# Performance work log

Hardware: AMD Instinct MI355X
Metric: run time of the kernel (lower is better)

The kernel has to match this reference:

```python
import jax, jax.numpy as jnp
import numpy as np

B, H, W, D = 64, 32, 32, 64
K = 1024  # codebook_size


def setup_inputs() -> dict:
    key = jax.random.key(0)
    kz, ke = jax.random.split(key)
    z = jax.random.normal(kz, (B, H, W, D), dtype=jnp.float32)
    embeddings = 0.02 * jax.random.normal(ke, (K, D), dtype=jnp.float32)
    return {"z": z, "embeddings": embeddings}


def reference(z, embeddings):
    # Flatten spatial/batch dims: (N, D) with N = B*H*W
    z_flat = z.reshape(-1, z.shape[-1])
    # Squared euclidean distances via ||a||^2 + ||b||^2 - 2 a.b  -> (N, K)
    distances = (jnp.sum(z_flat ** 2, axis=1, keepdims=True)
                 + jnp.sum(embeddings ** 2, axis=1)
                 - 2.0 * jnp.dot(z_flat, embeddings.T))
    indices = jnp.argmin(distances, axis=1)  # (N,)
    quantized = embeddings[indices].reshape(z.shape)  # (B, H, W, D)
    indices = indices.reshape(z.shape[0], z.shape[1], z.shape[2])  # (B, H, W)
    return quantized, indices
```

## Files before the change

kernel.cpp:

```cpp
#include <hip/hip_runtime.h>

#define NPTS   65536
#define DDIM   64
#define KCODES 1024
#define QOUT_ELEMS (NPTS * DDIM)

typedef _Float16 half8    __attribute__((ext_vector_type(8)));
typedef float    floatx16 __attribute__((ext_vector_type(16)));
typedef unsigned int uint;

#define AS1 __attribute__((address_space(1)))
#define AS3 __attribute__((address_space(3)))

#define WS_EHP   0
#define WS_ELP   (128*1024)
#define WS_E2    (256*1024)
#define WS_SCR   (264*1024)

union H8U { half8 v; uint u[4]; };

static __device__ __forceinline__ void gl_lds16(const void* g, void* l) {
    __builtin_amdgcn_global_load_lds((const AS1 uint*)g, (AS3 uint*)l, 16, 0, 0);
}

__global__ void eprep_kernel(const float* __restrict__ emb, char* __restrict__ ws) {
    const int tid = threadIdx.x;
    const int w = tid >> 6, d = tid & 63;
    const int k = blockIdx.x * 4 + w;
    float v = emb[(size_t)k * DDIM + d];
    _Float16 h = (_Float16)v;
    _Float16 l = (_Float16)(v - (float)h);
    size_t off = (size_t)(k >> 5) * 4096 + (size_t)(d >> 3) * 512
               + (size_t)(k & 31) * 16 + (size_t)(d & 7) * 2;
    *(_Float16*)(ws + WS_EHP + off) = h;
    *(_Float16*)(ws + WS_ELP + off) = l;
    float s = v * v;
    #pragma unroll
    for (int m = 1; m < 64; m <<= 1) s += __shfl_xor(s, m, 64);
    if (d == 0) {
        _Float16 e2h = (_Float16)s;
        _Float16 e2l = (_Float16)(s - (float)e2h);
        unsigned short hb = *(unsigned short*)&e2h;
        unsigned short lb = *(unsigned short*)&e2l;
        ((uint*)(ws + WS_E2))[k] = (uint)hb | ((uint)lb << 16);
    }
}

__global__ __launch_bounds__(256, 3) void vq_kernel(
    const float* __restrict__ z,
    const char* __restrict__ ws_c,
    float2* __restrict__ scr)
{
    const int tid  = threadIdx.x;
    const int lane = tid & 63;
    const int w    = __builtin_amdgcn_readfirstlane(tid >> 6);
    const int col  = lane & 31;
    const int sel8 = lane >> 5;
    const int pgrp = blockIdx.x >> 2;
    const int kq   = blockIdx.x & 3;

    __shared__ uint4 ldsbuf[2][512];
    __shared__ uint  lds_e2[256];

    const int pt = pgrp * 128 + w * 32 + col;
    half8 ah[4], al[4];
    {
        const float* zrow = z + (size_t)pt * DDIM + sel8 * 8;
        #pragma unroll
        for (int ks = 0; ks < 4; ++ks) {
            float4 u0 = *(const float4*)(zrow + ks * 16);
            float4 u1 = *(const float4*)(zrow + ks * 16 + 4);
            float tv[8] = {u0.x, u0.y, u0.z, u0.w, u1.x, u1.y, u1.z, u1.w};
            #pragma unroll
            for (int j = 0; j < 8; ++j) {
                float a = -2.0f * tv[j];
                _Float16 hh = (_Float16)a;
                ah[ks][j] = hh;
                al[ks][j] = (_Float16)(a - (float)hh);
            }
        }
    }
    half8 ahE;
    { H8U t0; t0.u[0] = (sel8 == 0) ? 0x3C003C00u : 0u;
      t0.u[1] = t0.u[2] = t0.u[3] = 0u; ahE = t0.v; }

    if (w == 0)
        gl_lds16(ws_c + WS_E2 + kq * 1024 + lane * 16, (char*)lds_e2);
    {
        const int opnd = w >> 1, hf = w & 1;
        const char* src = ws_c + (opnd ? WS_ELP : WS_EHP)
                        + (size_t)(kq * 8) * 4096 + hf * 2048 + lane * 16;
        char* dst = (char*)ldsbuf[0] + opnd * 4096 + hf * 2048;
        gl_lds16(src, dst);
        gl_lds16(src + 1024, dst + 1024);
    }

    const floatx16 zeroC = {};
    float best[16];
    int   bt[16];
    #pragma unroll
    for (int r = 0; r < 16; ++r) { best[r] = 3.4e38f; bt[r] = 0; }

    for (int t = 0; t < 8; ++t) {
        __syncthreads();
        if (t < 7) {
            const int opnd = w >> 1, hf = w & 1;
            const char* src = ws_c + (opnd ? WS_ELP : WS_EHP)
                            + (size_t)(kq * 8 + t + 1) * 4096 + hf * 2048 + lane * 16;
            char* dst = (char*)ldsbuf[(t + 1) & 1] + opnd * 4096 + hf * 2048;
            gl_lds16(src, dst);
            gl_lds16(src + 1024, dst + 1024);
        }
        const char* buf = (const char*)ldsbuf[t & 1];
        const char* ehb = buf + sel8 * 512 + col * 16;
        const char* elb = ehb + 4096;
        half8 bh[4], bl[4];
        #pragma unroll
        for (int ks = 0; ks < 4; ++ks) {
            bh[ks] = *(const half8*)(ehb + ks * 1024);
            bl[ks] = *(const half8*)(elb + ks * 1024);
        }
        half8 bhE;
        { H8U u; u.u[0] = lds_e2[t * 32 + col];
          u.u[1] = u.u[2] = u.u[3] = 0u; bhE = u.v; }

        floatx16 acc;
        acc = __builtin_amdgcn_mfma_f32_32x32x16_f16(ah[0], bh[0], zeroC, 0, 0, 0);
        acc = __builtin_amdgcn_mfma_f32_32x32x16_f16(ah[1], bh[1], acc, 0, 0, 0);
        acc = __builtin_amdgcn_mfma_f32_32x32x16_f16(ah[2], bh[2], acc, 0, 0, 0);
        acc = __builtin_amdgcn_mfma_f32_32x32x16_f16(ah[3], bh[3], acc, 0, 0, 0);
        acc = __builtin_amdgcn_mfma_f32_32x32x16_f16(ahE,  bhE,  acc, 0, 0, 0);
        acc = __builtin_amdgcn_mfma_f32_32x32x16_f16(ah[0], bl[0], acc, 0, 0, 0);
        acc = __builtin_amdgcn_mfma_f32_32x32x16_f16(ah[1], bl[1], acc, 0, 0, 0);
        acc = __builtin_amdgcn_mfma_f32_32x32x16_f16(ah[2], bl[2], acc, 0, 0, 0);
        acc = __builtin_amdgcn_mfma_f32_32x32x16_f16(ah[3], bl[3], acc, 0, 0, 0);
        acc = __builtin_amdgcn_mfma_f32_32x32x16_f16(al[0], bh[0], acc, 0, 0, 0);
        acc = __builtin_amdgcn_mfma_f32_32x32x16_f16(al[1], bh[1], acc, 0, 0, 0);
        acc = __builtin_amdgcn_mfma_f32_32x32x16_f16(al[2], bh[2], acc, 0, 0, 0);
        acc = __builtin_amdgcn_mfma_f32_32x32x16_f16(al[3], bh[3], acc, 0, 0, 0);

        #pragma unroll
        for (int r = 0; r < 16; ++r) {
            bool c = acc[r] < best[r];
            best[r] = c ? acc[r] : best[r];
            bt[r]   = c ? t      : bt[r];
        }
    }

    int code[16];
    #pragma unroll
    for (int r = 0; r < 16; ++r) code[r] = kq * 256 + bt[r] * 32 + col;
    #pragma unroll
    for (int m = 1; m < 32; m <<= 1) {
        #pragma unroll
        for (int r = 0; r < 16; ++r) {
            float ov = __shfl_xor(best[r], m, 64);
            int   oc = __shfl_xor(code[r], m, 64);
            bool c = (ov < best[r]) || (ov == best[r] && oc < code[r]);
            best[r] = c ? ov : best[r];
            code[r] = c ? oc : code[r];
        }
    }
    if (col == 0) {
        #pragma unroll
        for (int r = 0; r < 16; ++r) {
            int row = (r & 3) + 8 * (r >> 2) + 4 * sel8;
            int p = pgrp * 128 + w * 32 + row;
            scr[(size_t)p * 4 + kq] = make_float2(best[r], __int_as_float(code[r]));
        }
    }
}

__global__ void merge_gather_kernel(const float* __restrict__ emb,
                                    const float2* __restrict__ scr,
                                    float* __restrict__ out)
{
    int f = blockIdx.x * 256 + threadIdx.x;
    int pt = f >> 4, d4 = f & 15;
    float2 c0 = scr[(size_t)pt * 4];
    float bv = c0.x; int bi = __float_as_int(c0.y);
    #pragma unroll
    for (int j = 1; j < 4; ++j) {
        float2 cj = scr[(size_t)pt * 4 + j];
        if (cj.x < bv) { bv = cj.x; bi = __float_as_int(cj.y); }
    }
    ((float4*)out)[(size_t)pt * 16 + d4] = ((const float4*)emb)[(size_t)bi * 16 + d4];
    if (d4 == 0) out[QOUT_ELEMS + pt] = (float)bi;
}

extern "C" void kernel_launch(void* const* d_in, const int* in_sizes, int n_in,
                              void* d_out, int out_size, void* d_ws, size_t ws_size,
                              hipStream_t stream) {
    const float* z   = (const float*)d_in[0];
    const float* emb = (const float*)d_in[1];
    float* out = (float*)d_out;
    char* ws = (char*)d_ws;
    float2* scr = (float2*)(ws + WS_SCR);

    eprep_kernel<<<KCODES / 4, 256, 0, stream>>>(emb, ws);
    vq_kernel<<<2048, 256, 0, stream>>>(z, ws, scr);
    merge_gather_kernel<<<NPTS * 16 / 256, 256, 0, stream>>>(emb, scr, out);
}
```

Before: 118.0 us.

## Swap MFMA operand roles: keep codebook slice in registers, stream points through LDS

A new zprep kernel pre-splits -2z into fp16 hi/lo pairs in an MFMA-friendly tiled layout. The main kernel now holds a 128-code slice of the codebook in registers and streams 256 points through double-buffered LDS, not the other way round. The ||e||^2 term becomes a plain fp32 register add instead of an extra MFMA. The argmin is now reduced inside each thread's accumulator rows, with one cross-half shuffle and an LDS merge across waves, replacing the 5-step shuffle reduction. The cost is an extra pass that writes and rereads 16 MB of z halves, an 8-way candidate merge per point, and a reworked gather kernel.

Result: no change. 117.8 us (-0.2%).

```diff
diff --git a/kernel.cpp b/kernel.cpp
--- a/kernel.cpp
+++ b/kernel.cpp
@@ -14,10 +14,10 @@
 
 #define WS_EHP   0
 #define WS_ELP   (128*1024)
-#define WS_E2    (256*1024)
-#define WS_SCR   (264*1024)
-
-union H8U { half8 v; uint u[4]; };
+#define WS_E2F   (256*1024)
+#define WS_ZH    (512*1024)
+#define WS_ZL    (WS_ZH + 8*1024*1024)
+#define WS_SCR   (WS_ZH + 16*1024*1024)
 
 static __device__ __forceinline__ void gl_lds16(const void* g, void* l) {
     __builtin_amdgcn_global_load_lds((const AS1 uint*)g, (AS3 uint*)l, 16, 0, 0);
@@ -37,17 +37,23 @@
     float s = v * v;
     #pragma unroll
     for (int m = 1; m < 64; m <<= 1) s += __shfl_xor(s, m, 64);
-    if (d == 0) {
-        _Float16 e2h = (_Float16)s;
-        _Float16 e2l = (_Float16)(s - (float)e2h);
-        unsigned short hb = *(unsigned short*)&e2h;
-        unsigned short lb = *(unsigned short*)&e2l;
-        ((uint*)(ws + WS_E2))[k] = (uint)hb | ((uint)lb << 16);
-    }
+    if (d == 0) ((float*)(ws + WS_E2F))[k] = s;
+}
+
+__global__ void zprep_kernel(const float* __restrict__ z, char* __restrict__ ws) {
+    const int tid = threadIdx.x;
+    const int w = tid >> 6, d = tid & 63;
+    const int p = blockIdx.x * 4 + w;
+    float a = -2.0f * z[(size_t)p * DDIM + d];
+    _Float16 h = (_Float16)a;
+    _Float16 l = (_Float16)(a - (float)h);
+    size_t off = (size_t)(p >> 5) * 4096 + (size_t)(d >> 3) * 512
+               + (size_t)(p & 31) * 16 + (size_t)(d & 7) * 2;
+    *(_Float16*)(ws + WS_ZH + off) = h;
+    *(_Float16*)(ws + WS_ZL + off) = l;
 }
 
 __global__ __launch_bounds__(256, 3) void vq_kernel(
-    const float* __restrict__ z,
     const char* __restrict__ ws_c,
     float2* __restrict__ scr)
 {
@@ -56,80 +62,76 @@
     const int w    = __builtin_amdgcn_readfirstlane(tid >> 6);
     const int col  = lane & 31;
     const int sel8 = lane >> 5;
-    const int pgrp = blockIdx.x >> 2;
-    const int kq   = blockIdx.x & 3;
-
-    __shared__ uint4 ldsbuf[2][512];
-    __shared__ uint  lds_e2[256];
-
-    const int pt = pgrp * 128 + w * 32 + col;
+    const int pgrp = blockIdx.x >> 3;
+    const int kg   = blockIdx.x & 7;
+
+    __shared__ uint4  zbuf[2][512];
+    __shared__ float2 cand[2][4][32];
+
+    const char* eb = ws_c + WS_EHP + (size_t)(kg * 4 + w) * 4096 + sel8 * 512 + col * 16;
     half8 ah[4], al[4];
+    #pragma unroll
+    for (int ks = 0; ks < 4; ++ks) {
+        ah[ks] = *(const half8*)(eb + ks * 1024);
+        al[ks] = *(const half8*)(eb + (WS_ELP - WS_EHP) + ks * 1024);
+    }
+    float e2r[16];
     {
-        const float* zrow = z + (size_t)pt * DDIM + sel8 * 8;
-        #pragma unroll
-        for (int ks = 0; ks < 4; ++ks) {
-            float4 u0 = *(const float4*)(zrow + ks * 16);
-            float4 u1 = *(const float4*)(zrow + ks * 16 + 4);
-            float tv[8] = {u0.x, u0.y, u0.z, u0.w, u1.x, u1.y, u1.z, u1.w};
-            #pragma unroll
-            for (int j = 0; j < 8; ++j) {
-                float a = -2.0f * tv[j];
-                _Float16 hh = (_Float16)a;
-                ah[ks][j] = hh;
-                al[ks][j] = (_Float16)(a - (float)hh);
-            }
-        }
-    }
-    half8 ahE;
-    { H8U t0; t0.u[0] = (sel8 == 0) ? 0x3C003C00u : 0u;
-      t0.u[1] = t0.u[2] = t0.u[3] = 0u; ahE = t0.v; }
-
-    if (w == 0)
-        gl_lds16(ws_c + WS_E2 + kq * 1024 + lane * 16, (char*)lds_e2);
+        const float* e2f = (const float*)(ws_c + WS_E2F) + kg * 128 + w * 32 + 4 * sel8;
+        #pragma unroll
+        for (int r = 0; r < 16; ++r)
+            e2r[r] = e2f[(r & 3) + 8 * (r >> 2)];
+    }
+
     {
         const int opnd = w >> 1, hf = w & 1;
-        const char* src = ws_c + (opnd ? WS_ELP : WS_EHP)
-                        + (size_t)(kq * 8) * 4096 + hf * 2048 + lane * 16;
-        char* dst = (char*)ldsbuf[0] + opnd * 4096 + hf * 2048;
+        const char* src = ws_c + (opnd ? WS_ZL : WS_ZH)
+                        + (size_t)(pgrp * 8) * 4096 + hf * 2048 + lane * 16;
+        char* dst = (char*)zbuf[0] + opnd * 4096 + hf * 2048;
         gl_lds16(src, dst);
         gl_lds16(src + 1024, dst + 1024);
     }
 
     const floatx16 zeroC = {};
-    float best[16];
-    int   bt[16];
-    #pragma unroll
-    for (int r = 0; r < 16; ++r) { best[r] = 3.4e38f; bt[r] = 0; }
 
     for (int t = 0; t < 8; ++t) {
         __syncthreads();
         if (t < 7) {
             const int opnd = w >> 1, hf = w & 1;
-            const char* src = ws_c + (opnd ? WS_ELP : WS_EHP)
-                            + (size_t)(kq * 8 + t + 1) * 4096 + hf * 2048 + lane * 16;
-            char* dst = (char*)ldsbuf[(t + 1) & 1] + opnd * 4096 + hf * 2048;
+            const char* src = ws_c + (opnd ? WS_ZL : WS_ZH)
+                            + (size_t)(pgrp * 8 + t + 1) * 4096 + hf * 2048 + lane * 16;
+            char* dst = (char*)zbuf[(t + 1) & 1] + opnd * 4096 + hf * 2048;
             gl_lds16(src, dst);
             gl_lds16(src + 1024, dst + 1024);
         }
-        const char* buf = (const char*)ldsbuf[t & 1];
-        const char* ehb = buf + sel8 * 512 + col * 16;
-        const char* elb = ehb + 4096;
+        if (t > 0 && w == ((t - 1) & 3) && lane < 32) {
+            const int tt = t - 1;
+            float2 c0 = cand[tt & 1][0][lane];
+            float bvm = c0.x; int bim = __float_as_int(c0.y);
+            #pragma unroll
+            for (int j = 1; j < 4; ++j) {
+                float2 cj = cand[tt & 1][j][lane];
+                bool c = cj.x < bvm;
+                bvm = c ? cj.x : bvm;
+                bim = c ? __float_as_int(cj.y) : bim;
+            }
+            int ptg = (pgrp * 8 + tt) * 32 + lane;
+            scr[(size_t)ptg * 8 + kg] = make_float2(bvm, __int_as_float(bim));
+        }
+
+        const char* zb = (const char*)zbuf[t & 1] + sel8 * 512 + col * 16;
         half8 bh[4], bl[4];
         #pragma unroll
         for (int ks = 0; ks < 4; ++ks) {
-            bh[ks] = *(const half8*)(ehb + ks * 1024);
-            bl[ks] = *(const half8*)(elb + ks * 1024);
-        }
-        half8 bhE;
-        { H8U u; u.u[0] = lds_e2[t * 32 + col];
-          u.u[1] = u.u[2] = u.u[3] = 0u; bhE = u.v; }
+            bh[ks] = *(const half8*)(zb + ks * 1024);
+            bl[ks] = *(const half8*)(zb + 4096 + ks * 1024);
+        }
 
         floatx16 acc;
         acc = __builtin_amdgcn_mfma_f32_32x32x16_f16(ah[0], bh[0], zeroC, 0, 0, 0);
         acc = __builtin_amdgcn_mfma_f32_32x32x16_f16(ah[1], bh[1], acc, 0, 0, 0);
         acc = __builtin_amdgcn_mfma_f32_32x32x16_f16(ah[2], bh[2], acc, 0, 0, 0);
         acc = __builtin_amdgcn_mfma_f32_32x32x16_f16(ah[3], bh[3], acc, 0, 0, 0);
-        acc = __builtin_amdgcn_mfma_f32_32x32x16_f16(ahE,  bhE,  acc, 0, 0, 0);
         acc = __builtin_amdgcn_mfma_f32_32x32x16_f16(ah[0], bl[0], acc, 0, 0, 0);
         acc = __builtin_amdgcn_mfma_f32_32x32x16_f16(ah[1], bl[1], acc, 0, 0, 0);
         acc = __builtin_amdgcn_mfma_f32_32x32x16_f16(ah[2], bl[2], acc, 0, 0, 0);
@@ -139,35 +141,38 @@
         acc = __builtin_amdgcn_mfma_f32_32x32x16_f16(al[2], bh[2], acc, 0, 0, 0);
         acc = __builtin_amdgcn_mfma_f32_32x32x16_f16(al[3], bh[3], acc, 0, 0, 0);
 
-        #pragma unroll
-        for (int r = 0; r < 16; ++r) {
-            bool c = acc[r] < best[r];
-            best[r] = c ? acc[r] : best[r];
-            bt[r]   = c ? t      : bt[r];
-        }
-    }
-
-    int code[16];
-    #pragma unroll
-    for (int r = 0; r < 16; ++r) code[r] = kq * 256 + bt[r] * 32 + col;
-    #pragma unroll
-    for (int m = 1; m < 32; m <<= 1) {
-        #pragma unroll
-        for (int r = 0; r < 16; ++r) {
-            float ov = __shfl_xor(best[r], m, 64);
-            int   oc = __shfl_xor(code[r], m, 64);
-            bool c = (ov < best[r]) || (ov == best[r] && oc < code[r]);
-            best[r] = c ? ov : best[r];
-            code[r] = c ? oc : code[r];
-        }
-    }
-    if (col == 0) {
-        #pragma unroll
-        for (int r = 0; r < 16; ++r) {
-            int row = (r & 3) + 8 * (r >> 2) + 4 * sel8;
-            int p = pgrp * 128 + w * 32 + row;
-            scr[(size_t)p * 4 + kq] = make_float2(best[r], __int_as_float(code[r]));
-        }
+        float sc[16];
+        #pragma unroll
+        for (int r = 0; r < 16; ++r) sc[r] = acc[r] + e2r[r];
+        float bv = sc[0]; int br = 0;
+        #pragma unroll
+        for (int r = 1; r < 16; ++r) {
+            bool c = sc[r] < bv;
+            bv = c ? sc[r] : bv;
+            br = c ? r : br;
+        }
+        int bc = kg * 128 + w * 32 + (br & 3) + 8 * (br >> 2) + 4 * sel8;
+        float ov = __shfl_xor(bv, 32, 64);
+        int   oc = __shfl_xor(bc, 32, 64);
+        bool cm = (ov < bv) || (ov == bv && oc < bc);
+        bv = cm ? ov : bv;
+        bc = cm ? oc : bc;
+        if (lane < 32) cand[t & 1][w][lane] = make_float2(bv, __int_as_float(bc));
+    }
+
+    __syncthreads();
+    if (w == 3 && lane < 32) {
+        float2 c0 = cand[1][0][lane];
+        float bvm = c0.x; int bim = __float_as_int(c0.y);
+        #pragma unroll
+        for (int j = 1; j < 4; ++j) {
+            float2 cj = cand[1][j][lane];
+            bool c = cj.x < bvm;
+            bvm = c ? cj.x : bvm;
+            bim = c ? __float_as_int(cj.y) : bim;
+        }
+        int ptg = (pgrp * 8 + 7) * 32 + lane;
+        scr[(size_t)ptg * 8 + kg] = make_float2(bvm, __int_as_float(bim));
     }
 }
 
@@ -175,17 +180,27 @@
                                     const float2* __restrict__ scr,
                                     float* __restrict__ out)
 {
-    int f = blockIdx.x * 256 + threadIdx.x;
-    int pt = f >> 4, d4 = f & 15;
-    float2 c0 = scr[(size_t)pt * 4];
-    float bv = c0.x; int bi = __float_as_int(c0.y);
-    #pragma unroll
-    for (int j = 1; j < 4; ++j) {
-        float2 cj = scr[(size_t)pt * 4 + j];
-        if (cj.x < bv) { bv = cj.x; bi = __float_as_int(cj.y); }
-    }
-    ((float4*)out)[(size_t)pt * 16 + d4] = ((const float4*)emb)[(size_t)bi * 16 + d4];
-    if (d4 == 0) out[QOUT_ELEMS + pt] = (float)bi;
+    __shared__ int s_idx[16];
+    const int tid = threadIdx.x;
+    if (tid < 16) {
+        int pt = blockIdx.x * 16 + tid;
+        const float2* c = scr + (size_t)pt * 8;
+        float bv = c[0].x; int bi = __float_as_int(c[0].y);
+        #pragma unroll
+        for (int j = 1; j < 8; ++j) {
+            float2 cj = c[j];
+            bool cc = cj.x < bv;
+            bv = cc ? cj.x : bv;
+            bi = cc ? __float_as_int(cj.y) : bi;
+        }
+        s_idx[tid] = bi;
+        out[QOUT_ELEMS + pt] = (float)bi;
+    }
+    __syncthreads();
+    int p = tid >> 4, d4 = tid & 15;
+    int ks = s_idx[p];
+    ((float4*)out)[((size_t)blockIdx.x * 16 + p) * 16 + d4] =
+        ((const float4*)emb)[(size_t)ks * 16 + d4];
 }
 
 extern "C" void kernel_launch(void* const* d_in, const int* in_sizes, int n_in,
@@ -198,6 +213,7 @@
     float2* scr = (float2*)(ws + WS_SCR);
 
     eprep_kernel<<<KCODES / 4, 256, 0, stream>>>(emb, ws);
-    vq_kernel<<<2048, 256, 0, stream>>>(z, ws, scr);
-    merge_gather_kernel<<<NPTS * 16 / 256, 256, 0, stream>>>(emb, scr, out);
-}
+    zprep_kernel<<<NPTS / 4, 256, 0, stream>>>(z, ws);
+    vq_kernel<<<2048, 256, 0, stream>>>(ws, scr);
+    merge_gather_kernel<<<NPTS / 16, 256, 0, stream>>>(emb, scr, out);
+}
```
